# Optimization experiments

Hardware: AMD Instinct MI355X
Metric: run time of the kernel (lower is better)

Reference implementation:

```python
import jax, jax.numpy as jnp
import numpy as np

N, E, D, H, C, ED = 50000, 800000, 128, 2, 128, 8
LEAKY_SLOPE = 0.2
SOFTMAX_EPS = 1e-16
LN_EPS = 1e-5


def setup_inputs() -> dict:
    key = jax.random.key(0)
    ks = jax.random.split(key, 12)
    s = lambda k, shp, scale: jax.random.normal(k, shp, dtype=jnp.float32) * scale
    return {
        "x": s(ks[0], (N, D), 1.0),
        "edge_index": jax.random.randint(ks[1], (2, E), 0, N, dtype=jnp.int64),
        "edge_attr": s(ks[2], (E, ED), 1.0),
        "W_ep": s(ks[3], (ED, D), 1.0 / np.sqrt(ED)),
        "b_ep": jnp.zeros((D,), jnp.float32),
        "W_lin": s(ks[4], (D, H * C), 1.0 / np.sqrt(D)),
        "att_src": s(ks[5], (H, C), 1.0 / np.sqrt(C)),
        "att_dst": s(ks[6], (H, C), 1.0 / np.sqrt(C)),
        "W_le": s(ks[7], (D, H * C), 1.0 / np.sqrt(D)),
        "att_edge": s(ks[8], (H, C), 1.0 / np.sqrt(C)),
        "bias_gat": jnp.zeros((C,), jnp.float32),
        "ln_gamma": jnp.ones((C,), jnp.float32),
        "ln_beta": jnp.zeros((C,), jnp.float32),
    }


def reference(x, edge_index, edge_attr, W_ep, b_ep, W_lin, att_src, att_dst,
              W_le, att_edge, bias_gat, ln_gamma, ln_beta):
    src, dst = edge_index[0], edge_index[1]
    # edge_proj: [E, ED] -> [E, D]
    e = edge_attr @ W_ep + b_ep
    # node projection: [N, H, C]
    h = (x @ W_lin).reshape(N, H, C)
    # edge projection inside GATConv: [E, H, C]
    ee = (e @ W_le).reshape(E, H, C)
    # attention logits
    a_src = jnp.einsum('nhc,hc->nh', h, att_src)      # [N, H]
    a_dst = jnp.einsum('nhc,hc->nh', h, att_dst)      # [N, H]
    a_edge = jnp.einsum('ehc,hc->eh', ee, att_edge)   # [E, H]
    score = a_src[src] + a_dst[dst] + a_edge          # [E, H]
    score = jnp.where(score >= 0, score, LEAKY_SLOPE * score)
    # segment softmax over incoming edges of each dst node
    smax = jax.ops.segment_max(score, dst, num_segments=N)     # [N, H]
    ex = jnp.exp(score - smax[dst])
    denom = jax.ops.segment_sum(ex, dst, num_segments=N)       # [N, H]
    alpha = ex / (denom[dst] + SOFTMAX_EPS)                    # [E, H]
    # message + scatter-add aggregation
    msg = h[src] * alpha[:, :, None]                           # [E, H, C]
    agg = jax.ops.segment_sum(msg, dst, num_segments=N)        # [N, H, C]
    out = agg.mean(axis=1) + bias_gat                          # concat=False -> head mean
    # residual + LayerNorm (dropout = identity in eval mode)
    y = out + x
    mu = y.mean(axis=-1, keepdims=True)
    var = y.var(axis=-1, keepdims=True)
    return (y - mu) * jax.lax.rsqrt(var + LN_EPS) * ln_gamma + ln_beta
```

## Files before the change

kernel.cpp:

```cpp
#include <hip/hip_runtime.h>
#include <hip/hip_bf16.h>

#define NN 50000
#define EE 800000
#define DD 128
#define HH 2
#define CC 128
#define HC 256
#define EDD 8

#define LEAKY 0.2f
#define SMEPS 1e-16f
#define LNEPS 1e-5f

#define SCAN_B 196
#define CONV_B 3125
#define K2_B   782

#define HB_OFF    0u
#define ASRC_OFF  25600000u
#define ADST_OFF  26000000u
#define CONST_OFF 26400000u
#define SD_OFF    26404096u
#define CNT_OFF   32804096u
#define ROW_OFF   33004800u
#define PAY_OFF   33205504u
#define WBT_OFF   39605504u
#define BSUM_OFF  39671040u

typedef __attribute__((ext_vector_type(8))) short short8v;
typedef __attribute__((ext_vector_type(4))) float float4v;
typedef __attribute__((ext_vector_type(2))) int int2v;

__device__ __forceinline__ float bf2f(unsigned short v) {
  return __uint_as_float(((unsigned)v) << 16);
}
__device__ __forceinline__ unsigned short f2bf(float f) {
  __hip_bfloat16 b = __float2bfloat16(f);
  return *reinterpret_cast<unsigned short*>(&b);
}

__global__ __launch_bounds__(256) void kA_prep_convert(const float* __restrict__ W_lin,
                                                       const float* __restrict__ att_src,
                                                       const float* __restrict__ att_dst,
                                                       const float* __restrict__ W_le,
                                                       const float* __restrict__ att_edge,
                                                       const float* __restrict__ W_ep,
                                                       const float* __restrict__ b_ep,
                                                       const int* __restrict__ ei_raw,
                                                       float* __restrict__ consts,
                                                       unsigned short* __restrict__ wbT,
                                                       int* __restrict__ cnt,
                                                       int2v* __restrict__ sd) {
  int b = blockIdx.x, tid = threadIdx.x;
  if (b == 0) {
    __shared__ float vlds[HH * DD];
    int h = tid >> 7, d = tid & 127;
    const float* as = att_src + h * CC;
    const float* ad = att_dst + h * CC;
    const float* ae = att_edge + h * CC;
    float us = 0.f, ud = 0.f, vv = 0.f;
    for (int c = 0; c < CC; ++c) {
      float wl = W_lin[d * HC + h * CC + c];
      float we = W_le[d * HC + h * CC + c];
      us += wl * as[c]; ud += wl * ad[c]; vv += we * ae[c];
    }
    consts[h * 128 + d] = us;
    consts[256 + h * 128 + d] = ud;
    vlds[h * 128 + d] = vv;
    __syncthreads();
    if (tid < 16) {
      int hh = tid >> 3, k = tid & 7;
      float w = 0.f;
      for (int dd2 = 0; dd2 < DD; ++dd2) w += W_ep[k * DD + dd2] * vlds[hh * 128 + dd2];
      consts[512 + hh * 8 + k] = w;
    }
    if (tid < 2) {
      float ce = 0.f;
      for (int dd2 = 0; dd2 < DD; ++dd2) ce += b_ep[dd2] * vlds[tid * 128 + dd2];
      consts[528 + tid] = ce;
    }
  } else if (b <= 128) {
    int i = (b - 1) * 256 + tid;
    int k = i >> 8, c = i & 255;
    wbT[c * DD + k] = f2bf(W_lin[i]);
  } else {
    int lane = threadIdx.x & 63;
    int probe = ei_raw[2 * lane + 1];
    bool is64 = (__ballot(probe != 0) == 0ull);
    int i = (b - 129) * 256 + tid;
    int s, d;
    if (is64) { s = ei_raw[2 * i]; d = ei_raw[2 * (EE + i)]; }
    else      { s = ei_raw[i];     d = ei_raw[EE + i]; }
    int rk = atomicAdd(&cnt[d], 1);
    int2v v; v.x = s; v.y = d | (rk << 16);
    sd[i] = v;
  }
}

__global__ __launch_bounds__(256) void k_scan1(const int* __restrict__ cnt,
                                               int* __restrict__ rowstart,
                                               int* __restrict__ bsum) {
  __shared__ int sp[256];
  int t = threadIdx.x, b = blockIdx.x;
  int n = b * 256 + t;
  int v = (n < NN) ? cnt[n] : 0;
  sp[t] = v;
  __syncthreads();
  for (int off = 1; off < 256; off <<= 1) {
    int u = (t >= off) ? sp[t - off] : 0;
    __syncthreads();
    sp[t] += u;
    __syncthreads();
  }
  if (n < NN) rowstart[n] = sp[t] - v;
  if (t == 255) bsum[b] = sp[255];
}

__global__ __launch_bounds__(256) void kB_scan_mfma(int* __restrict__ rowstart,
                                                    const int* __restrict__ bsum,
                                                    const float* __restrict__ x,
                                                    const unsigned short* __restrict__ wbT,
                                                    const float* __restrict__ consts,
                                                    unsigned char* __restrict__ hbuf8,
                                                    float* __restrict__ a_src,
                                                    float* __restrict__ a_dst) {
  __shared__ unsigned short xs[64 * 256];
  int tid = threadIdx.x;

  if (blockIdx.x < SCAN_B) {
    int* sp = (int*)xs;
    int t = tid, b = blockIdx.x;
    int v = (t < SCAN_B) ? bsum[t] : 0;
    sp[t] = v;
    __syncthreads();
    for (int off = 1; off < 256; off <<= 1) {
      int u = (t >= off) ? sp[t - off] : 0;
      __syncthreads();
      sp[t] += u;
      __syncthreads();
    }
    int boff = (b == 0) ? 0 : sp[b - 1];
    int n = b * 256 + t;
    if (n < NN) rowstart[n] += boff;
    if (n == NN) rowstart[NN] = EE;
    return;
  }

  int n0 = (blockIdx.x - SCAN_B) * 64;
  int r = tid >> 2, q = tid & 3;
  int n = n0 + r;
  bool valid = (n < NN);

  float xv[32];
  const float4* xp = (const float4*)(x + (size_t)n * DD + q * 32);
#pragma unroll
  for (int j = 0; j < 8; ++j) {
    float4 v = valid ? xp[j] : make_float4(0.f, 0.f, 0.f, 0.f);
    xv[j * 4 + 0] = v.x; xv[j * 4 + 1] = v.y; xv[j * 4 + 2] = v.z; xv[j * 4 + 3] = v.w;
  }
  float ps0 = 0.f, ps1 = 0.f, pd0 = 0.f, pd1 = 0.f;
#pragma unroll
  for (int j = 0; j < 32; j += 4) {
    float4 u0 = *(const float4*)(consts +   0 + q * 32 + j);
    float4 u1 = *(const float4*)(consts + 128 + q * 32 + j);
    float4 v0 = *(const float4*)(consts + 256 + q * 32 + j);
    float4 v1 = *(const float4*)(consts + 384 + q * 32 + j);
    ps0 += xv[j] * u0.x + xv[j+1] * u0.y + xv[j+2] * u0.z + xv[j+3] * u0.w;
    ps1 += xv[j] * u1.x + xv[j+1] * u1.y + xv[j+2] * u1.z + xv[j+3] * u1.w;
    pd0 += xv[j] * v0.x + xv[j+1] * v0.y + xv[j+2] * v0.z + xv[j+3] * v0.w;
    pd1 += xv[j] * v1.x + xv[j+1] * v1.y + xv[j+2] * v1.z + xv[j+3] * v1.w;
  }
#pragma unroll
  for (int off = 1; off < 4; off <<= 1) {
    ps0 += __shfl_xor(ps0, off); ps1 += __shfl_xor(ps1, off);
    pd0 += __shfl_xor(pd0, off); pd1 += __shfl_xor(pd1, off);
  }
  if (q == 0 && valid) {
    *(float2*)(a_src + n * 2) = make_float2(ps0, ps1);
    *(float2*)(a_dst + n * 2) = make_float2(pd0, pd1);
  }

#pragma unroll
  for (int ci = 0; ci < 4; ++ci) {
    union { short8v v; unsigned short u[8]; } pk;
#pragma unroll
    for (int j = 0; j < 8; ++j) pk.u[j] = f2bf(xv[ci * 8 + j]);
    unsigned byte = r * 256 + (q * 4 + ci) * 16;
    byte ^= (r & 7) << 4;
    *(short8v*)((char*)xs + byte) = pk.v;
  }

  int wave = tid >> 6, l = tid & 63;
  int wc = wave * 64;
  int lr = l & 15, lg = l >> 4;
  short8v bfr[4][4];
#pragma unroll
  for (int ct = 0; ct < 4; ++ct) {
    int col = wc + ct * 16 + lr;
#pragma unroll
    for (int kt = 0; kt < 4; ++kt)
      bfr[ct][kt] = *(const short8v*)(wbT + (size_t)col * DD + kt * 32 + lg * 8);
  }

  __syncthreads();

  float4v acc[4][4];
#pragma unroll
  for (int rt = 0; rt < 4; ++rt)
#pragma unroll
    for (int ct = 0; ct < 4; ++ct) acc[rt][ct] = (float4v){0.f, 0.f, 0.f, 0.f};

#pragma unroll
  for (int kt = 0; kt < 4; ++kt) {
    short8v afr[4];
#pragma unroll
    for (int rt = 0; rt < 4; ++rt) {
      int row = rt * 16 + lr;
      unsigned byte = row * 256 + kt * 64 + lg * 16;
      byte ^= (row & 7) << 4;
      afr[rt] = *(const short8v*)((const char*)xs + byte);
    }
#pragma unroll
    for (int rt = 0; rt < 4; ++rt)
#pragma unroll
      for (int ct = 0; ct < 4; ++ct)
        acc[rt][ct] = __builtin_amdgcn_mfma_f32_16x16x32_bf16(afr[rt], bfr[ct][kt], acc[rt][ct], 0, 0, 0);
  }

  __syncthreads();
#pragma unroll
  for (int rt = 0; rt < 4; ++rt) {
#pragma unroll
    for (int j = 0; j < 4; ++j) {
      int row = rt * 16 + lg * 4 + j;
#pragma unroll
      for (int ct = 0; ct < 4; ++ct) {
        int col = wc + ct * 16 + lr;
        int idx2 = ((col & 127) << 1) | (col >> 7);
        unsigned o = (unsigned)idx2 * 2;
        unsigned byte = row * 512 + (o ^ ((((unsigned)(row & 7) ^ ((o >> 7) & 3))) << 4));
        *(unsigned short*)((char*)xs + byte) = f2bf(acc[rt][ct][j]);
      }
    }
  }
  __syncthreads();
  {
    int r2 = tid >> 2, q2 = tid & 3;
    int n2 = n0 + r2;
    if (n2 < NN) {
#pragma unroll
      for (int kk = 0; kk < 4; ++kk) {
        unsigned u4[4];
#pragma unroll
        for (int t2 = 0; t2 < 2; ++t2) {
          int k = kk * 2 + t2;
          unsigned o = q2 * 128 + k * 16;
          unsigned byte = r2 * 512 + (o ^ ((((unsigned)(r2 & 7) ^ ((o >> 7) & 3))) << 4));
          short8v v = *(short8v*)((char*)xs + byte);
          unsigned ua = __builtin_amdgcn_cvt_pk_fp8_f32(bf2f((unsigned short)v[0]), bf2f((unsigned short)v[1]), 0u, false);
          ua = __builtin_amdgcn_cvt_pk_fp8_f32(bf2f((unsigned short)v[2]), bf2f((unsigned short)v[3]), ua, true);
          unsigned ub = __builtin_amdgcn_cvt_pk_fp8_f32(bf2f((unsigned short)v[4]), bf2f((unsigned short)v[5]), 0u, false);
          ub = __builtin_amdgcn_cvt_pk_fp8_f32(bf2f((unsigned short)v[6]), bf2f((unsigned short)v[7]), ub, true);
          u4[t2 * 2] = ua; u4[t2 * 2 + 1] = ub;
        }
        uint4 w4 = make_uint4(u4[0], u4[1], u4[2], u4[3]);
        *(uint4*)(hbuf8 + (size_t)n2 * 256 + q2 * 64 + kk * 16) = w4;
      }
    }
  }
}

__global__ __launch_bounds__(256) void k34_edge(const int2v* __restrict__ sd,
                                                const int* __restrict__ rowstart,
                                                const float* __restrict__ edge_attr,
                                                const float* __restrict__ a_src,
                                                const float* __restrict__ a_dst,
                                                const float* __restrict__ consts,
                                                int2v* __restrict__ payload) {
  int e = blockIdx.x * 256 + threadIdx.x;
  int2v sdv = sd[e];
  int s = sdv.x;
  unsigned y = (unsigned)sdv.y;
  int d = (int)(y & 0xFFFFu);
  int rk = (int)(y >> 16);
  float4 ea0 = *(const float4*)(edge_attr + (size_t)e * 8);
  float4 ea1 = *(const float4*)(edge_attr + (size_t)e * 8 + 4);
  float2 asv = *(const float2*)(a_src + s * 2);
  float2 adv = *(const float2*)(a_dst + d * 2);
  const float* w0 = consts + 512;
  const float* w1 = consts + 520;
  float sc0 = asv.x + adv.x + consts[528]
            + ea0.x * w0[0] + ea0.y * w0[1] + ea0.z * w0[2] + ea0.w * w0[3]
            + ea1.x * w0[4] + ea1.y * w0[5] + ea1.z * w0[6] + ea1.w * w0[7];
  float sc1 = asv.y + adv.y + consts[529]
            + ea0.x * w1[0] + ea0.y * w1[1] + ea0.z * w1[2] + ea0.w * w1[3]
            + ea1.x * w1[4] + ea1.y * w1[5] + ea1.z * w1[6] + ea1.w * w1[7];
  sc0 = (sc0 >= 0.f) ? sc0 : LEAKY * sc0;
  sc1 = (sc1 >= 0.f) ? sc1 : LEAKY * sc1;
  float ex0 = __expf(sc0);
  float ex1 = __expf(sc1);
  unsigned pk = (unsigned)f2bf(ex0) | ((unsigned)f2bf(ex1) << 16);
  int pos = rowstart[d] + rk;
  int2v pv; pv.x = s << 8; pv.y = (int)pk;
  payload[pos] = pv;
}

__global__ __launch_bounds__(256) void k5_fused(const int* __restrict__ rowstart,
                                                const int2v* __restrict__ payload,
                                                const unsigned char* __restrict__ hb8,
                                                const float* __restrict__ x,
                                                const float* __restrict__ bias,
                                                const float* __restrict__ gamma,
                                                const float* __restrict__ beta,
                                                float* __restrict__ out) {
  int n = blockIdx.x * 4 + (threadIdx.x >> 6);
  int lane = threadIdx.x & 63;
  if (n >= NN) return;
  int p0i = __builtin_amdgcn_readfirstlane(rowstart[n]);
  int p1i = __builtin_amdgcn_readfirstlane(rowstart[n + 1]);
  int len = p1i - p0i;
  int c0 = lane * 2;
  const int2v* pp = payload + p0i;
  float a00 = 0.f, a01 = 0.f, a10 = 0.f, a11 = 0.f, se0 = 0.f, se1 = 0.f;

#define K5_LD(soff) (*(const unsigned*)(hb8 + (size_t)(unsigned)(soff) + lane * 4))
#define K5_ACC(pl, w) { \
    float ex0 = bf2f((unsigned short)((unsigned)(pl).y & 0xffffu)); \
    float ex1 = bf2f((unsigned short)(((unsigned)(pl).y) >> 16)); \
    a00 = fmaf(ex0, __builtin_amdgcn_cvt_f32_fp8((int)(w), 0), a00); \
    a01 = fmaf(ex1, __builtin_amdgcn_cvt_f32_fp8((int)(w), 1), a01); \
    a10 = fmaf(ex0, __builtin_amdgcn_cvt_f32_fp8((int)(w), 2), a10); \
    a11 = fmaf(ex1, __builtin_amdgcn_cvt_f32_fp8((int)(w), 3), a11); \
    se0 += ex0; se1 += ex1; }

  if (len > 0) {
    int2v p0 = pp[0];
    int2v p1 = (len > 1) ? pp[1] : p0;
    int2v p2 = (len > 2) ? pp[2] : p0;
    int2v p3 = (len > 3) ? pp[3] : p0;
    unsigned h0 = K5_LD(p0.x), h1 = K5_LD(p1.x), h2 = K5_LD(p2.x), h3 = K5_LD(p3.x);
    int i = 0;
    for (; i + 7 < len; i += 4) {
      int2v q0 = pp[i + 4], q1 = pp[i + 5], q2 = pp[i + 6], q3 = pp[i + 7];
      unsigned g0 = K5_LD(q0.x), g1 = K5_LD(q1.x), g2 = K5_LD(q2.x), g3 = K5_LD(q3.x);
      K5_ACC(p0, h0); K5_ACC(p1, h1); K5_ACC(p2, h2); K5_ACC(p3, h3);
      p0 = q0; p1 = q1; p2 = q2; p3 = q3;
      h0 = g0; h1 = g1; h2 = g2; h3 = g3;
    }
    int r = len - i;
    K5_ACC(p0, h0);
    if (r > 1) K5_ACC(p1, h1);
    if (r > 2) K5_ACC(p2, h2);
    if (r > 3) K5_ACC(p3, h3);
    if (r > 4) {
      int rem = r - 4;
      int2v q0 = pp[i + 4];
      int2v q1 = (rem > 1) ? pp[i + 5] : q0;
      int2v q2 = (rem > 2) ? pp[i + 6] : q0;
      unsigned g0 = K5_LD(q0.x), g1 = K5_LD(q1.x), g2 = K5_LD(q2.x);
      K5_ACC(q0, g0);
      if (rem > 1) K5_ACC(q1, g1);
      if (rem > 2) K5_ACC(q2, g2);
    }
  }
#undef K5_LD
#undef K5_ACC

  float inv0 = 0.5f / (se0 + SMEPS);
  float inv1 = 0.5f / (se1 + SMEPS);
  float2 xv = *(const float2*)(x + (size_t)n * DD + c0);
  float v0 = a00 * inv0 + a01 * inv1 + bias[c0] + xv.x;
  float v1 = a10 * inv0 + a11 * inv1 + bias[c0 + 1] + xv.y;
  float s = v0 + v1, ss = v0 * v0 + v1 * v1;
#pragma unroll
  for (int o = 32; o > 0; o >>= 1) {
    s += __shfl_xor(s, o);
    ss += __shfl_xor(ss, o);
  }
  float mu = s * (1.f / 128.f);
  float var = ss * (1.f / 128.f) - mu * mu;
  float rstd = rsqrtf(var + LNEPS);
  float2 ov;
  ov.x = (v0 - mu) * rstd * gamma[c0] + beta[c0];
  ov.y = (v1 - mu) * rstd * gamma[c0 + 1] + beta[c0 + 1];
  *(float2*)(out + (size_t)n * CC + c0) = ov;
}

extern "C" void kernel_launch(void* const* d_in, const int* in_sizes, int n_in,
                              void* d_out, int out_size, void* d_ws, size_t ws_size,
                              hipStream_t stream) {
  const float* x        = (const float*)d_in[0];
  const int*   ei_raw   = (const int*)d_in[1];
  const float* edge_attr= (const float*)d_in[2];
  const float* W_ep     = (const float*)d_in[3];
  const float* b_ep     = (const float*)d_in[4];
  const float* W_lin    = (const float*)d_in[5];
  const float* att_src  = (const float*)d_in[6];
  const float* att_dst  = (const float*)d_in[7];
  const float* W_le     = (const float*)d_in[8];
  const float* att_edge = (const float*)d_in[9];
  const float* bias_gat = (const float*)d_in[10];
  const float* ln_gamma = (const float*)d_in[11];
  const float* ln_beta  = (const float*)d_in[12];

  char* ws = (char*)d_ws;
  unsigned char* hbuf8 = (unsigned char*)(ws + HB_OFF);
  float*    a_src  = (float*)(ws + ASRC_OFF);
  float*    a_dst  = (float*)(ws + ADST_OFF);
  float*    consts = (float*)(ws + CONST_OFF);
  int2v*    sd     = (int2v*)(ws + SD_OFF);
  int*      cnt    = (int*)(ws + CNT_OFF);
  int*      rowst  = (int*)(ws + ROW_OFF);
  int2v*    payload= (int2v*)(ws + PAY_OFF);
  unsigned short* wbT = (unsigned short*)(ws + WBT_OFF);
  int*      bsum   = (int*)(ws + BSUM_OFF);

  hipMemsetAsync(cnt, 0, (size_t)NN * 4, stream);
  kA_prep_convert<<<129 + CONV_B, 256, 0, stream>>>(W_lin, att_src, att_dst, W_le, att_edge,
                                                    W_ep, b_ep, ei_raw, consts, wbT, cnt, sd);
  k_scan1<<<SCAN_B, 256, 0, stream>>>(cnt, rowst, bsum);
  kB_scan_mfma<<<SCAN_B + K2_B, 256, 0, stream>>>(rowst, bsum, x, wbT, consts, hbuf8, a_src, a_dst);
  k34_edge<<<CONV_B, 256, 0, stream>>>(sd, rowst, edge_attr, a_src, a_dst, consts, payload);
  k5_fused<<<(NN + 3) / 4, 256, 0, stream>>>(rowst, payload, hbuf8, x, bias_gat, ln_gamma, ln_beta, (float*)d_out);
}
```

Before: 145.9 us.

## Split in-degree counters per XCD to keep histogram atomics local

Replaces the single global per-destination counter array with eight copies, one per XCD, read from the hardware XCC_ID register. The counting atomics become workgroup-scoped so they can resolve in the XCD-local L2 instead of crossing dies. The scan kernels then sum the eight counts to build per-XCD base offsets, and the edge kernel places each edge using its XCD's base. This adds eight times the counter memory and extra scan traffic, and relies on workgroup-scope atomics being coherent across all CUs in one XCD, which the HIP memory model does not guarantee.

```diff
diff --git a/kernel.cpp b/kernel.cpp
--- a/kernel.cpp
+++ b/kernel.cpp
@@ -16,17 +16,19 @@
 #define SCAN_B 196
 #define CONV_B 3125
 #define K2_B   782
+#define NPAD   50176
 
 #define HB_OFF    0u
-#define ASRC_OFF  25600000u
-#define ADST_OFF  26000000u
-#define CONST_OFF 26400000u
-#define SD_OFF    26404096u
-#define CNT_OFF   32804096u
-#define ROW_OFF   33004800u
-#define PAY_OFF   33205504u
-#define WBT_OFF   39605504u
-#define BSUM_OFF  39671040u
+#define ASRC_OFF  12800000u
+#define ADST_OFF  13200000u
+#define CONST_OFF 13600000u
+#define SD_OFF    13604096u
+#define CNT8_OFF  20004096u
+#define ROW_OFF   21609728u
+#define BASE8_OFF 21810432u
+#define PAY_OFF   23416064u
+#define WBT_OFF   29816064u
+#define BSUM_OFF  29881600u
 
 typedef __attribute__((ext_vector_type(8))) short short8v;
 typedef __attribute__((ext_vector_type(4))) float float4v;
@@ -50,7 +52,7 @@
                                                        const int* __restrict__ ei_raw,
                                                        float* __restrict__ consts,
                                                        unsigned short* __restrict__ wbT,
-                                                       int* __restrict__ cnt,
+                                                       int* __restrict__ cnt8,
                                                        int2v* __restrict__ sd) {
   int b = blockIdx.x, tid = threadIdx.x;
   if (b == 0) {
@@ -88,24 +90,33 @@
     int lane = threadIdx.x & 63;
     int probe = ei_raw[2 * lane + 1];
     bool is64 = (__ballot(probe != 0) == 0ull);
+    int xcd = __builtin_amdgcn_s_getreg((20) | (0 << 6) | ((32 - 1) << 11)) & 7;
     int i = (b - 129) * 256 + tid;
     int s, d;
     if (is64) { s = ei_raw[2 * i]; d = ei_raw[2 * (EE + i)]; }
     else      { s = ei_raw[i];     d = ei_raw[EE + i]; }
-    int rk = atomicAdd(&cnt[d], 1);
-    int2v v; v.x = s; v.y = d | (rk << 16);
+    int rk = __hip_atomic_fetch_add(&cnt8[xcd * NPAD + d], 1,
+                                    __ATOMIC_RELAXED, __HIP_MEMORY_SCOPE_WORKGROUP);
+    int2v v; v.x = s; v.y = d | (rk << 16) | (xcd << 29);
     sd[i] = v;
   }
 }
 
-__global__ __launch_bounds__(256) void k_scan1(const int* __restrict__ cnt,
+__global__ __launch_bounds__(256) void k_scan1(const int* __restrict__ cnt8,
                                                int* __restrict__ rowstart,
+                                               int* __restrict__ base8,
                                                int* __restrict__ bsum) {
   __shared__ int sp[256];
   int t = threadIdx.x, b = blockIdx.x;
   int n = b * 256 + t;
-  int v = (n < NN) ? cnt[n] : 0;
-  sp[t] = v;
+  int c[8];
+  int tot = 0;
+#pragma unroll
+  for (int r = 0; r < 8; ++r) {
+    c[r] = (n < NN) ? cnt8[r * NPAD + n] : 0;
+    tot += c[r];
+  }
+  sp[t] = tot;
   __syncthreads();
   for (int off = 1; off < 256; off <<= 1) {
     int u = (t >= off) ? sp[t - off] : 0;
@@ -113,12 +124,19 @@
     sp[t] += u;
     __syncthreads();
   }
-  if (n < NN) rowstart[n] = sp[t] - v;
+  int intra = sp[t] - tot;
+  if (n < NN) {
+    rowstart[n] = intra;
+    int run = intra;
+#pragma unroll
+    for (int r = 0; r < 8; ++r) { base8[r * NPAD + n] = run; run += c[r]; }
+  }
   if (t == 255) bsum[b] = sp[255];
 }
 
 __global__ __launch_bounds__(256) void kB_scan_mfma(int* __restrict__ rowstart,
                                                     const int* __restrict__ bsum,
+                                                    int* __restrict__ base8,
                                                     const float* __restrict__ x,
                                                     const unsigned short* __restrict__ wbT,
                                                     const float* __restrict__ consts,
@@ -142,7 +160,11 @@
     }
     int boff = (b == 0) ? 0 : sp[b - 1];
     int n = b * 256 + t;
-    if (n < NN) rowstart[n] += boff;
+    if (n < NN) {
+      rowstart[n] += boff;
+#pragma unroll
+      for (int r = 0; r < 8; ++r) base8[r * NPAD + n] += boff;
+    }
     if (n == NN) rowstart[NN] = EE;
     return;
   }
@@ -272,7 +294,7 @@
 }
 
 __global__ __launch_bounds__(256) void k34_edge(const int2v* __restrict__ sd,
-                                                const int* __restrict__ rowstart,
+                                                const int* __restrict__ base8,
                                                 const float* __restrict__ edge_attr,
                                                 const float* __restrict__ a_src,
                                                 const float* __restrict__ a_dst,
@@ -283,7 +305,8 @@
   int s = sdv.x;
   unsigned y = (unsigned)sdv.y;
   int d = (int)(y & 0xFFFFu);
-  int rk = (int)(y >> 16);
+  int rk = (int)((y >> 16) & 0x1FFFu);
+  int xcd = (int)(y >> 29);
   float4 ea0 = *(const float4*)(edge_attr + (size_t)e * 8);
   float4 ea1 = *(const float4*)(edge_attr + (size_t)e * 8 + 4);
   float2 asv = *(const float2*)(a_src + s * 2);
@@ -301,7 +324,7 @@
   float ex0 = __expf(sc0);
   float ex1 = __expf(sc1);
   unsigned pk = (unsigned)f2bf(ex0) | ((unsigned)f2bf(ex1) << 16);
-  int pos = rowstart[d] + rk;
+  int pos = base8[xcd * NPAD + d] + rk;
   int2v pv; pv.x = s << 8; pv.y = (int)pk;
   payload[pos] = pv;
 }
@@ -410,17 +433,18 @@
   float*    a_dst  = (float*)(ws + ADST_OFF);
   float*    consts = (float*)(ws + CONST_OFF);
   int2v*    sd     = (int2v*)(ws + SD_OFF);
-  int*      cnt    = (int*)(ws + CNT_OFF);
+  int*      cnt8   = (int*)(ws + CNT8_OFF);
   int*      rowst  = (int*)(ws + ROW_OFF);
+  int*      base8  = (int*)(ws + BASE8_OFF);
   int2v*    payload= (int2v*)(ws + PAY_OFF);
   unsigned short* wbT = (unsigned short*)(ws + WBT_OFF);
   int*      bsum   = (int*)(ws + BSUM_OFF);
 
-  hipMemsetAsync(cnt, 0, (size_t)NN * 4, stream);
+  hipMemsetAsync(cnt8, 0, (size_t)8 * NPAD * 4, stream);
   kA_prep_convert<<<129 + CONV_B, 256, 0, stream>>>(W_lin, att_src, att_dst, W_le, att_edge,
-                                                    W_ep, b_ep, ei_raw, consts, wbT, cnt, sd);
-  k_scan1<<<SCAN_B, 256, 0, stream>>>(cnt, rowst, bsum);
-  kB_scan_mfma<<<SCAN_B + K2_B, 256, 0, stream>>>(rowst, bsum, x, wbT, consts, hbuf8, a_src, a_dst);
-  k34_edge<<<CONV_B, 256, 0, stream>>>(sd, rowst, edge_attr, a_src, a_dst, consts, payload);
+                                                    W_ep, b_ep, ei_raw, consts, wbT, cnt8, sd);
+  k_scan1<<<SCAN_B, 256, 0, stream>>>(cnt8, rowst, base8, bsum);
+  kB_scan_mfma<<<SCAN_B + K2_B, 256, 0, stream>>>(rowst, bsum, base8, x, wbT, consts, hbuf8, a_src, a_dst);
+  k34_edge<<<CONV_B, 256, 0, stream>>>(sd, base8, edge_attr, a_src, a_dst, consts, payload);
   k5_fused<<<(NN + 3) / 4, 256, 0, stream>>>(rowst, payload, hbuf8, x, bias_gat, ln_gamma, ln_beta, (float*)d_out);
 }
```

Result: faster. 139.7 us (-4.3%).
